# Optimization experiments

Hardware: AMD Instinct MI355X
Metric: run time of the kernel (lower is better)

## Reference

```python
import jax, jax.numpy as jnp
import numpy as np

N_SRC = 100000
N_DST = 50000
N_EDGES = 800000
D = 128
D_OUT = 128


def setup_inputs() -> dict:
    key = jax.random.key(0)
    ks = jax.random.split(key, 8)
    H_src = jax.random.normal(ks[0], (N_SRC, D), dtype=jnp.float32)
    H_dst = jax.random.normal(ks[1], (N_DST, D), dtype=jnp.float32)
    HBar_src = jax.random.normal(ks[2], (N_SRC, D), dtype=jnp.float32)
    agg_HBar_dst = jax.random.normal(ks[3], (N_DST, D), dtype=jnp.float32)
    src_idx = jax.random.randint(ks[4], (N_EDGES,), 0, N_SRC, dtype=jnp.int64)
    dst_idx = jax.random.randint(ks[5], (N_EDGES,), 0, N_DST, dtype=jnp.int64)
    # Linear(in_feats*2, out_feats): store as [2D, D_OUT] for x @ W + b
    gain = float(np.sqrt(2.0))  # calculate_gain('relu')
    bound = gain * float(np.sqrt(6.0 / (2 * D + D_OUT)))  # xavier_uniform
    W = jax.random.uniform(ks[6], (2 * D, D_OUT), dtype=jnp.float32,
                           minval=-bound, maxval=bound)
    b = jnp.zeros((D_OUT,), dtype=jnp.float32)
    return {"H_src": H_src, "H_dst": H_dst, "HBar_src": HBar_src,
            "agg_HBar_dst": agg_HBar_dst, "W": W, "b": b,
            "src_idx": src_idx, "dst_idx": dst_idx}


def reference(H_src, H_dst, HBar_src, agg_HBar_dst, W, b, src_idx, dst_idx):
    # training path of SAGEConvWithCV: copy_u('hdelta') + mean over dst
    hdelta = H_src - HBar_src                      # [N_src, D]
    msgs = jnp.take(hdelta, src_idx, axis=0)       # [E, D] gather
    summed = jax.ops.segment_sum(msgs, dst_idx, num_segments=N_DST)  # [N_dst, D]
    deg = jax.ops.segment_sum(jnp.ones((src_idx.shape[0],), dtype=H_src.dtype),
                              dst_idx, num_segments=N_DST)           # [N_dst]
    hdelta_new = summed / jnp.maximum(deg, 1.0)[:, None]  # mean (0 for isolated)
    h_neigh = agg_HBar_dst + hdelta_new
    h = jnp.concatenate([H_dst, h_neigh], axis=1) @ W + b  # [N_dst, D_OUT]
    return jax.nn.relu(h)
```

## Files before the change

### kernel.cpp

```cpp
#include <hip/hip_runtime.h>
#include <hip/hip_bf16.h>
#include <cstdint>
#include <cstddef>

#define NSRC 100000
#define NDST 50000
#define DOUT 128
#define KK2 256
#define NBUCK 196
#define CHUNK 4096

typedef __attribute__((ext_vector_type(8))) short bf16x8;
typedef __attribute__((ext_vector_type(4))) float f32x4;
typedef __attribute__((ext_vector_type(2))) float f32x2;

static __device__ __forceinline__ unsigned short f2bf(float f) {
    union { float f; uint32_t u; } v; v.f = f;
    uint32_t u = v.u;
    uint32_t r = u + 0x7FFFu + ((u >> 16) & 1u);
    return (unsigned short)(r >> 16);
}

__global__ __launch_bounds__(256) void k_all1(const float4* __restrict__ a,
                                              const float4* __restrict__ b,
                                              uint32_t* __restrict__ o, int n4,
                                              const int* __restrict__ dst,
                                              int* __restrict__ part,
                                              const float* __restrict__ W,
                                              unsigned short* __restrict__ WT,
                                              int E, int nbe) {
    __shared__ int bh[NBUCK];
    int t = threadIdx.x;
    int bid = blockIdx.x;
    if (bid < nbe) {
        if (t < NBUCK) bh[t] = 0;
        __syncthreads();
        int base = bid * CHUNK;
        for (int i = t; i < CHUNK; i += 256) {
            int e = base + i;
            if (e < E) atomicAdd(&bh[dst[e] >> 8], 1);
        }
        __syncthreads();
        part[bid * 256 + t] = (t < NBUCK) ? bh[t] : 0;
    } else if (bid < nbe + 128) {
        int i = (bid - nbe) * 256 + t;
        int n = i >> 8, k = i & 255;
        WT[i] = f2bf(W[k * DOUT + n]);
    } else {
        int i = (bid - nbe - 128) * 256 + t;
        if (i < n4) {
            float4 x = a[i], y = b[i];
            uint32_t p = __builtin_amdgcn_cvt_pk_fp8_f32(x.x - y.x, x.y - y.y, 0u, false);
            p = __builtin_amdgcn_cvt_pk_fp8_f32(x.z - y.z, x.w - y.w, p, true);
            o[i] = p;
        }
    }
}

__global__ __launch_bounds__(256) void k_binA2(const int* __restrict__ src,
                                               const int* __restrict__ dst,
                                               const int* __restrict__ part,
                                               uint32_t* __restrict__ pairs,
                                               int E, int nbe) {
    __shared__ int lcur[NBUCK];
    __shared__ int wsum[4], wex[4];
    int t = threadIdx.x, lane = t & 63, w = t >> 6;
    int bid = blockIdx.x;

    int tot = 0, pre = 0;
    for (int j = 0; j < nbe; ++j) {
        int p = part[j * 256 + t];
        pre += (j < bid) ? p : 0;
        tot += p;
    }
    int v = (t < NBUCK) ? tot : 0;
    int x = v;
#pragma unroll
    for (int s = 1; s < 64; s <<= 1) { int tt = __shfl_up(x, s, 64); if (lane >= s) x += tt; }
    if (lane == 63) wsum[w] = x;
    __syncthreads();
    if (t == 0) {
        int run = 0;
#pragma unroll
        for (int k = 0; k < 4; ++k) { wex[k] = run; run += wsum[k]; }
    }
    __syncthreads();
    int ex = wex[w] + x - v;
    if (t < NBUCK) lcur[t] = ex + pre;
    __syncthreads();

    int base = bid * CHUNK;
    for (int i = t; i < CHUNK; i += 256) {
        int e = base + i;
        if (e < E) {
            int d = dst[e];
            int pos = atomicAdd(&lcur[d >> 8], 1);
            pairs[pos] = ((uint32_t)(d & 255) << 24) | (uint32_t)src[e];
        }
    }
}

__global__ __launch_bounds__(256) void k_binB(const uint32_t* __restrict__ pairs,
                                              const int* __restrict__ part,
                                              int* __restrict__ off,
                                              int* __restrict__ idx,
                                              int E, int nbe) {
    __shared__ int lcnt[256];
    __shared__ int lcur[256];
    __shared__ int wsum[4], wex[4];
    __shared__ int gbase_s, cnt_s;
    int b = blockIdx.x, t = threadIdx.x;
    int lane = t & 63, w = t >> 6;

    int tot = 0;
    for (int j = 0; j < nbe; ++j) tot += part[j * 256 + t];
    int v = (t < NBUCK) ? tot : 0;
    int x = v;
#pragma unroll
    for (int s = 1; s < 64; s <<= 1) { int tt = __shfl_up(x, s, 64); if (lane >= s) x += tt; }
    if (lane == 63) wsum[w] = x;
    __syncthreads();
    if (t == 0) {
        int run = 0;
#pragma unroll
        for (int k = 0; k < 4; ++k) { wex[k] = run; run += wsum[k]; }
    }
    __syncthreads();
    if (t == b) { gbase_s = wex[w] + x - v; cnt_s = tot; }
    lcnt[t] = 0;
    __syncthreads();
    int gbase = gbase_s;
    int cnt = cnt_s;

    for (int i = t; i < cnt; i += 256)
        atomicAdd(&lcnt[pairs[gbase + i] >> 24], 1);
    __syncthreads();

    v = lcnt[t];
    x = v;
#pragma unroll
    for (int s = 1; s < 64; s <<= 1) { int tt = __shfl_up(x, s, 64); if (lane >= s) x += tt; }
    if (lane == 63) wsum[w] = x;
    __syncthreads();
    if (t == 0) {
        int run = 0;
#pragma unroll
        for (int k = 0; k < 4; ++k) { wex[k] = run; run += wsum[k]; }
    }
    __syncthreads();
    int ex = wex[w] + x - v;
    lcur[t] = ex;
    int d = b * 256 + t;
    if (d < NDST) off[d] = gbase + ex;
    if (b == 0 && t == 0) off[NDST] = E;
    __syncthreads();

    for (int i = t; i < cnt; i += 256) {
        uint32_t p = pairs[gbase + i];
        int pos = atomicAdd(&lcur[p >> 24], 1);
        idx[gbase + pos] = (int)(p & 0xFFFFFFu);
    }
}

__global__ __launch_bounds__(256) void k_gath(const uint2* __restrict__ hd2,
                                              const float4* __restrict__ agg4,
                                              const int* __restrict__ off,
                                              const int* __restrict__ idx,
                                              bf16x8* __restrict__ Xn, int n) {
    int r = blockIdx.x * 4 + (threadIdx.x >> 6);
    if (r >= n) return;
    int lane = threadIdx.x & 63;
    int li = lane & 15, q = lane >> 4;
    float a0 = 0.f, a1 = 0.f, a2 = 0.f, a3 = 0.f;
    float a4 = 0.f, a5 = 0.f, a6 = 0.f, a7 = 0.f;
    int o0 = off[r], o1 = off[r + 1];
    for (int c = o0; c < o1; c += 64) {
        int m = o1 - c; if (m > 64) m = 64;
        int myi = (lane < m) ? idx[c + lane] : 0;
        for (int j = 0; j < m; j += 32) {
            int t0 = j + q,      t1 = j + 4 + q,  t2 = j + 8 + q,  t3 = j + 12 + q;
            int t4 = j + 16 + q, t5 = j + 20 + q, t6 = j + 24 + q, t7 = j + 28 + q;
            int s0 = __shfl(myi, t0), s1 = __shfl(myi, t1);
            int s2 = __shfl(myi, t2), s3 = __shfl(myi, t3);
            int s4 = __shfl(myi, t4), s5 = __shfl(myi, t5);
            int s6 = __shfl(myi, t6), s7 = __shfl(myi, t7);
            uint2 u0 = hd2[(size_t)s0 * 16 + li];
            uint2 u1 = hd2[(size_t)s1 * 16 + li];
            uint2 u2 = hd2[(size_t)s2 * 16 + li];
            uint2 u3 = hd2[(size_t)s3 * 16 + li];
            uint2 u4 = hd2[(size_t)s4 * 16 + li];
            uint2 u5 = hd2[(size_t)s5 * 16 + li];
            uint2 u6 = hd2[(size_t)s6 * 16 + li];
            uint2 u7 = hd2[(size_t)s7 * 16 + li];
            if (t0 >= m) { u0.x = 0; u0.y = 0; }
            if (t1 >= m) { u1.x = 0; u1.y = 0; }
            if (t2 >= m) { u2.x = 0; u2.y = 0; }
            if (t3 >= m) { u3.x = 0; u3.y = 0; }
            if (t4 >= m) { u4.x = 0; u4.y = 0; }
            if (t5 >= m) { u5.x = 0; u5.y = 0; }
            if (t6 >= m) { u6.x = 0; u6.y = 0; }
            if (t7 >= m) { u7.x = 0; u7.y = 0; }
#define ACC8(U) { \
            f32x2 lo0 = __builtin_amdgcn_cvt_pk_f32_fp8(U.x, false); \
            f32x2 hi0 = __builtin_amdgcn_cvt_pk_f32_fp8(U.x, true);  \
            f32x2 lo1 = __builtin_amdgcn_cvt_pk_f32_fp8(U.y, false); \
            f32x2 hi1 = __builtin_amdgcn_cvt_pk_f32_fp8(U.y, true);  \
            a0 += lo0[0]; a1 += lo0[1]; a2 += hi0[0]; a3 += hi0[1];  \
            a4 += lo1[0]; a5 += lo1[1]; a6 += hi1[0]; a7 += hi1[1];  }
            ACC8(u0) ACC8(u1) ACC8(u2) ACC8(u3)
            ACC8(u4) ACC8(u5) ACC8(u6) ACC8(u7)
#undef ACC8
        }
    }
    a0 += __shfl_xor(a0, 16); a1 += __shfl_xor(a1, 16);
    a2 += __shfl_xor(a2, 16); a3 += __shfl_xor(a3, 16);
    a4 += __shfl_xor(a4, 16); a5 += __shfl_xor(a5, 16);
    a6 += __shfl_xor(a6, 16); a7 += __shfl_xor(a7, 16);
    a0 += __shfl_xor(a0, 32); a1 += __shfl_xor(a1, 32);
    a2 += __shfl_xor(a2, 32); a3 += __shfl_xor(a3, 32);
    a4 += __shfl_xor(a4, 32); a5 += __shfl_xor(a5, 32);
    a6 += __shfl_xor(a6, 32); a7 += __shfl_xor(a7, 32);
    if (q == 0) {
        float inv = 1.0f / fmaxf((float)(o1 - o0), 1.0f);
        float4 g0 = agg4[(size_t)r * 32 + li * 2];
        float4 g1 = agg4[(size_t)r * 32 + li * 2 + 1];
        bf16x8 u;
        u[0] = (short)f2bf(g0.x + a0 * inv); u[1] = (short)f2bf(g0.y + a1 * inv);
        u[2] = (short)f2bf(g0.z + a2 * inv); u[3] = (short)f2bf(g0.w + a3 * inv);
        u[4] = (short)f2bf(g1.x + a4 * inv); u[5] = (short)f2bf(g1.y + a5 * inv);
        u[6] = (short)f2bf(g1.z + a6 * inv); u[7] = (short)f2bf(g1.w + a7 * inv);
        Xn[(size_t)r * 16 + li] = u;
    }
}

__global__ __launch_bounds__(256) void k_gemm(const float4* __restrict__ Hd4,
                                              const unsigned short* __restrict__ Xn,
                                              const unsigned short* __restrict__ WT,
                                              const float* __restrict__ bias,
                                              float* __restrict__ out) {
    __shared__ __align__(16) unsigned short xt[16][264];
    int r0 = blockIdx.x * 16;
    int t = threadIdx.x;

    {
#pragma unroll
        for (int p = 0; p < 2; ++p) {
            int f = t + p * 256;
            int row = f >> 5, c4 = f & 31;
            float4 v = Hd4[(size_t)(r0 + row) * 32 + c4];
            ushort4 u;
            u.x = f2bf(v.x); u.y = f2bf(v.y); u.z = f2bf(v.z); u.w = f2bf(v.w);
            *(ushort4*)&xt[row][c4 * 4] = u;
        }
        int row = t >> 4, col8 = (t & 15) * 8;
        bf16x8 xv = *reinterpret_cast<const bf16x8*>(Xn + (size_t)(r0 + row) * 128 + col8);
        *(bf16x8*)&xt[row][128 + col8] = xv;
    }
    __syncthreads();

    int w = t >> 6, lane = t & 63;
    int lr = lane & 15, lg = lane >> 4;
    const bf16x8* B0 = reinterpret_cast<const bf16x8*>(WT + (size_t)(w * 32 + lr) * KK2 + lg * 8);
    const bf16x8* B1 = reinterpret_cast<const bf16x8*>(WT + (size_t)(w * 32 + 16 + lr) * KK2 + lg * 8);

    f32x4 acc0 = {0.f, 0.f, 0.f, 0.f};
    f32x4 acc1 = {0.f, 0.f, 0.f, 0.f};
#pragma unroll
    for (int kk = 0; kk < 8; ++kk) {
        bf16x8 av = *reinterpret_cast<const bf16x8*>(&xt[lr][lg * 8 + kk * 32]);
        acc0 = __builtin_amdgcn_mfma_f32_16x16x32_bf16(av, B0[kk * 4], acc0, 0, 0, 0);
        acc1 = __builtin_amdgcn_mfma_f32_16x16x32_bf16(av, B1[kk * 4], acc1, 0, 0, 0);
    }

    int col0 = w * 32 + lr;
    int col1 = col0 + 16;
    float bi0 = bias[col0], bi1 = bias[col1];
    int rowb = r0 + lg * 4;
#pragma unroll
    for (int j = 0; j < 4; ++j) {
        float v0 = acc0[j] + bi0;
        float v1 = acc1[j] + bi1;
        out[(size_t)(rowb + j) * DOUT + col0] = v0 > 0.f ? v0 : 0.f;
        out[(size_t)(rowb + j) * DOUT + col1] = v1 > 0.f ? v1 : 0.f;
    }
}

extern "C" void kernel_launch(void* const* d_in, const int* in_sizes, int n_in,
                              void* d_out, int out_size, void* d_ws, size_t ws_size,
                              hipStream_t stream) {
    const float* H_src    = (const float*)d_in[0];
    const float* H_dst    = (const float*)d_in[1];
    const float* HBar_src = (const float*)d_in[2];
    const float* agg      = (const float*)d_in[3];
    const float* W        = (const float*)d_in[4];
    const float* bias     = (const float*)d_in[5];
    const int*   src      = (const int*)d_in[6];
    const int*   dst      = (const int*)d_in[7];
    float* out = (float*)d_out;
    const int E = in_sizes[6];

    char* ws = (char*)d_ws;
    int* part            = (int*)ws;
    int* off             = (int*)(ws + 200704);
    uint32_t* pairs      = (uint32_t*)(ws + 401408);
    int* idx_sorted      = (int*)(ws + 3601408);
    unsigned short* WT   = (unsigned short*)(ws + 6801408);
    unsigned short* hd8  = (unsigned short*)(ws + 6866944);
    unsigned short* Xn   = (unsigned short*)(ws + 19666944);

    const int NBE = (E + CHUNK - 1) / CHUNK;
    int n4 = NSRC * 32;
    int nStream = (n4 + 255) / 256;

    k_all1<<<NBE + 128 + nStream, 256, 0, stream>>>(
        (const float4*)H_src, (const float4*)HBar_src, (uint32_t*)hd8, n4,
        dst, part, W, WT, E, NBE);

    k_binA2<<<NBE, 256, 0, stream>>>(src, dst, part, pairs, E, NBE);
    k_binB<<<NBUCK, 256, 0, stream>>>(pairs, part, off, idx_sorted, E, NBE);

    k_gath<<<(NDST + 3) / 4, 256, 0, stream>>>(
        (const uint2*)hd8, (const float4*)agg, off, idx_sorted,
        (bf16x8*)Xn, NDST);

    k_gemm<<<NDST / 16, 256, 0, stream>>>(
        (const float4*)H_dst, Xn, WT, bias, out);
}
```

Before: 140.6 us.

## Replace per-chunk bucket partials with global atomic counts and atomic bucket cursors

The per-chunk histogram array, which later kernels scanned with a loop over all chunks, is replaced by a single global bucket count built with atomics. Bucket write offsets in the binning pass now come from an atomic cursor per bucket, after that pass recomputes its own chunk histogram. This removes the O(nbe) partial-sum loops in binA2 and binB. In exchange it adds an extra init kernel launch, global atomics, and a second histogram pass. Edge order within a bucket becomes nondeterministic, so the summation order can vary between runs.

```diff
diff --git a/kernel.cpp b/kernel.cpp
--- a/kernel.cpp
+++ b/kernel.cpp
@@ -21,33 +21,39 @@
     return (unsigned short)(r >> 16);
 }
 
-__global__ __launch_bounds__(256) void k_all1(const float4* __restrict__ a,
-                                              const float4* __restrict__ b,
-                                              uint32_t* __restrict__ o, int n4,
-                                              const int* __restrict__ dst,
-                                              int* __restrict__ part,
-                                              const float* __restrict__ W,
+__global__ __launch_bounds__(256) void k_prep(const float* __restrict__ W,
                                               unsigned short* __restrict__ WT,
-                                              int E, int nbe) {
+                                              int* __restrict__ bcnt,
+                                              int* __restrict__ bcur2) {
+    int i = blockIdx.x * 256 + threadIdx.x;
+    if (i < DOUT * KK2) {
+        int n = i >> 8;
+        int k = i & 255;
+        WT[i] = f2bf(W[k * DOUT + n]);
+    }
+    if (i < 256) { bcnt[i] = 0; bcur2[i] = 0; }
+}
+
+__global__ __launch_bounds__(256) void k_hd_binA1(const float4* __restrict__ a,
+                                                  const float4* __restrict__ b,
+                                                  uint32_t* __restrict__ o, int n4,
+                                                  const int* __restrict__ dst,
+                                                  int* __restrict__ bcnt,
+                                                  int E, int nbe) {
     __shared__ int bh[NBUCK];
     int t = threadIdx.x;
-    int bid = blockIdx.x;
-    if (bid < nbe) {
+    if ((int)blockIdx.x < nbe) {
         if (t < NBUCK) bh[t] = 0;
         __syncthreads();
-        int base = bid * CHUNK;
+        int base = blockIdx.x * CHUNK;
         for (int i = t; i < CHUNK; i += 256) {
             int e = base + i;
             if (e < E) atomicAdd(&bh[dst[e] >> 8], 1);
         }
         __syncthreads();
-        part[bid * 256 + t] = (t < NBUCK) ? bh[t] : 0;
-    } else if (bid < nbe + 128) {
-        int i = (bid - nbe) * 256 + t;
-        int n = i >> 8, k = i & 255;
-        WT[i] = f2bf(W[k * DOUT + n]);
+        if (t < NBUCK && bh[t]) atomicAdd(&bcnt[t], bh[t]);
     } else {
-        int i = (bid - nbe - 128) * 256 + t;
+        int i = ((int)blockIdx.x - nbe) * 256 + t;
         if (i < n4) {
             float4 x = a[i], y = b[i];
             uint32_t p = __builtin_amdgcn_cvt_pk_fp8_f32(x.x - y.x, x.y - y.y, 0u, false);
@@ -59,21 +65,23 @@
 
 __global__ __launch_bounds__(256) void k_binA2(const int* __restrict__ src,
                                                const int* __restrict__ dst,
-                                               const int* __restrict__ part,
-                                               uint32_t* __restrict__ pairs,
-                                               int E, int nbe) {
-    __shared__ int lcur[NBUCK];
+                                               const int* __restrict__ bcnt,
+                                               int* __restrict__ bcur2,
+                                               uint32_t* __restrict__ pairs, int E) {
+    __shared__ int bh[NBUCK], lcur[NBUCK];
     __shared__ int wsum[4], wex[4];
-    int t = threadIdx.x, lane = t & 63, w = t >> 6;
-    int bid = blockIdx.x;
-
-    int tot = 0, pre = 0;
-    for (int j = 0; j < nbe; ++j) {
-        int p = part[j * 256 + t];
-        pre += (j < bid) ? p : 0;
-        tot += p;
-    }
-    int v = (t < NBUCK) ? tot : 0;
+    int t = threadIdx.x;
+    int lane = t & 63, w = t >> 6;
+
+    if (t < NBUCK) bh[t] = 0;
+    __syncthreads();
+    int base = blockIdx.x * CHUNK;
+    for (int i = t; i < CHUNK; i += 256) {
+        int e = base + i;
+        if (e < E) atomicAdd(&bh[dst[e] >> 8], 1);
+    }
+
+    int v = (t < NBUCK) ? bcnt[t] : 0;
     int x = v;
 #pragma unroll
     for (int s = 1; s < 64; s <<= 1) { int tt = __shfl_up(x, s, 64); if (lane >= s) x += tt; }
@@ -86,10 +94,10 @@
     }
     __syncthreads();
     int ex = wex[w] + x - v;
-    if (t < NBUCK) lcur[t] = ex + pre;
-    __syncthreads();
-
-    int base = bid * CHUNK;
+
+    if (t < NBUCK) lcur[t] = bh[t] ? (ex + atomicAdd(&bcur2[t], bh[t])) : 0;
+    __syncthreads();
+
     for (int i = t; i < CHUNK; i += 256) {
         int e = base + i;
         if (e < E) {
@@ -101,20 +109,17 @@
 }
 
 __global__ __launch_bounds__(256) void k_binB(const uint32_t* __restrict__ pairs,
-                                              const int* __restrict__ part,
+                                              const int* __restrict__ bcnt,
                                               int* __restrict__ off,
-                                              int* __restrict__ idx,
-                                              int E, int nbe) {
+                                              int* __restrict__ idx, int E) {
     __shared__ int lcnt[256];
     __shared__ int lcur[256];
     __shared__ int wsum[4], wex[4];
-    __shared__ int gbase_s, cnt_s;
+    __shared__ int gbase_s;
     int b = blockIdx.x, t = threadIdx.x;
     int lane = t & 63, w = t >> 6;
 
-    int tot = 0;
-    for (int j = 0; j < nbe; ++j) tot += part[j * 256 + t];
-    int v = (t < NBUCK) ? tot : 0;
+    int v = (t < NBUCK) ? bcnt[t] : 0;
     int x = v;
 #pragma unroll
     for (int s = 1; s < 64; s <<= 1) { int tt = __shfl_up(x, s, 64); if (lane >= s) x += tt; }
@@ -126,11 +131,11 @@
         for (int k = 0; k < 4; ++k) { wex[k] = run; run += wsum[k]; }
     }
     __syncthreads();
-    if (t == b) { gbase_s = wex[w] + x - v; cnt_s = tot; }
+    if (t == b) gbase_s = wex[w] + x - v;
     lcnt[t] = 0;
     __syncthreads();
     int gbase = gbase_s;
-    int cnt = cnt_s;
+    int cnt = bcnt[b];
 
     for (int i = t; i < cnt; i += 256)
         atomicAdd(&lcnt[pairs[gbase + i] >> 24], 1);
@@ -300,24 +305,27 @@
     const int E = in_sizes[6];
 
     char* ws = (char*)d_ws;
-    int* part            = (int*)ws;
-    int* off             = (int*)(ws + 200704);
-    uint32_t* pairs      = (uint32_t*)(ws + 401408);
-    int* idx_sorted      = (int*)(ws + 3601408);
-    unsigned short* WT   = (unsigned short*)(ws + 6801408);
-    unsigned short* hd8  = (unsigned short*)(ws + 6866944);
-    unsigned short* Xn   = (unsigned short*)(ws + 19666944);
+    int* bcnt            = (int*)ws;
+    int* bcur2           = (int*)(ws + 1024);
+    int* off             = (int*)(ws + 3072);
+    uint32_t* pairs      = (uint32_t*)(ws + 203264);
+    int* idx_sorted      = (int*)(ws + 3403264);
+    unsigned short* WT   = (unsigned short*)(ws + 6603264);
+    unsigned short* hd8  = (unsigned short*)(ws + 6668800);
+    unsigned short* Xn   = (unsigned short*)(ws + 19468800);
 
     const int NBE = (E + CHUNK - 1) / CHUNK;
     int n4 = NSRC * 32;
     int nStream = (n4 + 255) / 256;
 
-    k_all1<<<NBE + 128 + nStream, 256, 0, stream>>>(
+    k_prep<<<128, 256, 0, stream>>>(W, WT, bcnt, bcur2);
+
+    k_hd_binA1<<<NBE + nStream, 256, 0, stream>>>(
         (const float4*)H_src, (const float4*)HBar_src, (uint32_t*)hd8, n4,
-        dst, part, W, WT, E, NBE);
-
-    k_binA2<<<NBE, 256, 0, stream>>>(src, dst, part, pairs, E, NBE);
-    k_binB<<<NBUCK, 256, 0, stream>>>(pairs, part, off, idx_sorted, E, NBE);
+        dst, bcnt, E, NBE);
+
+    k_binA2<<<NBE, 256, 0, stream>>>(src, dst, bcnt, bcur2, pairs, E);
+    k_binB<<<NBUCK, 256, 0, stream>>>(pairs, bcnt, off, idx_sorted, E);
 
     k_gath<<<(NDST + 3) / 4, 256, 0, stream>>>(
         (const uint2*)hd8, (const float4*)agg, off, idx_sorted,
```

Measured after the change: 116.5 us. 1.21x faster.
